# Kernel optimization log

Measured on AMD Instinct MI355X. Metric: run time of the kernel, lower is better.

## Reference

```python
import jax, jax.numpy as jnp
import numpy as np

N_QUBITS = 4
N_LAYERS = 2
BATCH = 262144


def _apply_ry(psi, theta, wire):
    # psi: (B, 2,2,2,2) real statevector; theta: scalar or (B,)
    c = jnp.reshape(jnp.cos(theta * 0.5), (-1, 1, 1, 1))
    s = jnp.reshape(jnp.sin(theta * 0.5), (-1, 1, 1, 1))
    psi = jnp.moveaxis(psi, wire + 1, 1)
    a, b = psi[:, 0], psi[:, 1]
    psi = jnp.stack([c * a - s * b, s * a + c * b], axis=1)
    return jnp.moveaxis(psi, 1, wire + 1)


def _apply_cnot(psi, ctrl, tgt):
    # flip target amplitude where control bit is 1
    psi = jnp.moveaxis(psi, (ctrl + 1, tgt + 1), (1, 2))
    psi = psi.at[:, 1].set(psi[:, 1, ::-1])
    return jnp.moveaxis(psi, (1, 2), (ctrl + 1, tgt + 1))


def _circuit(encoded, q_params):
    # Batched 4-qubit statevector sim (RY/CNOT are real matrices -> real psi).
    B = encoded.shape[0]
    psi = jnp.zeros((B, 2 ** N_QUBITS), encoded.dtype).at[:, 0].set(1.0)
    psi = psi.reshape((B,) + (2,) * N_QUBITS)  # wire 0 = most significant axis
    for w in range(N_QUBITS):
        psi = _apply_ry(psi, encoded[:, w], w)
    for layer in range(N_LAYERS):
        for i in range(N_QUBITS - 1):
            psi = _apply_cnot(psi, i, i + 1)
        psi = _apply_cnot(psi, N_QUBITS - 1, 0)  # ring closure (n_qubits > 2)
        for i in range(N_QUBITS):
            psi = _apply_ry(psi, q_params[layer * N_QUBITS + i], i)
    p = psi * psi  # probabilities
    zs = []
    for w in range(N_QUBITS):
        pw = jnp.moveaxis(p, w + 1, 1).reshape(B, 2, -1)
        zs.append(pw[:, 0].sum(-1) - pw[:, 1].sum(-1))  # <Z_w>
    return jnp.stack(zs, axis=-1)  # (B, 4)


def setup_inputs() -> dict:
    key = jax.random.key(0)
    ks = jax.random.split(key, 10)
    f32 = jnp.float32
    state = jax.random.normal(ks[0], (BATCH, 64), dtype=f32)
    # state_encoder: Linear(64,32) -> ReLU -> Linear(32,4) -> Tanh
    W1 = jax.random.normal(ks[1], (32, 64), dtype=f32) / np.sqrt(64.0)
    b1 = jnp.zeros((32,), f32)
    W2 = jax.random.normal(ks[2], (N_QUBITS, 32), dtype=f32) / np.sqrt(32.0)
    b2 = jnp.zeros((N_QUBITS,), f32)
    q_params = jax.random.normal(ks[3], (N_LAYERS * N_QUBITS,), dtype=f32) * 0.1
    # q_value_head: Linear(4,32) -> ReLU -> Linear(32,16) -> Tanh
    H1 = jax.random.normal(ks[4], (32, N_QUBITS), dtype=f32) / np.sqrt(float(N_QUBITS))
    c1 = jnp.zeros((32,), f32)
    H2 = jax.random.normal(ks[5], (16, 32), dtype=f32) / np.sqrt(32.0)
    c2 = jnp.zeros((16,), f32)
    return {"state": state, "W1": W1, "b1": b1, "W2": W2, "b2": b2,
            "q_params": q_params, "H1": H1, "c1": c1, "H2": H2, "c2": c2}


def reference(state, W1, b1, W2, b2, q_params, H1, c1, H2, c2):
    B = state.shape[0]
    x = state.reshape(B, -1)
    h = jax.nn.relu(x @ W1.T + b1)
    encoded = jnp.tanh(h @ W2.T + b2)            # (B, 4) rotation angles
    qf = _circuit(encoded, q_params)             # (B, 4) PauliZ expectations
    h2 = jax.nn.relu(qf @ H1.T + c1)
    q_values = jnp.tanh(h2 @ H2.T + c2)          # (B, 16)
    return q_values.reshape(B, 4, 4)
```

## Files before the change

kernel.cpp:

```cpp
#include <hip/hip_runtime.h>
#include <hip/hip_bf16.h>

#define TPB 256
#define BATCH 262144
#define S 34

typedef __fp16   fp16x2  __attribute__((ext_vector_type(2)));
typedef _Float16 half8_t __attribute__((ext_vector_type(8)));
typedef float    f32x4   __attribute__((ext_vector_type(4)));

#define WAVE_LDS_FENCE() asm volatile("s_waitcnt lgkmcnt(0)" ::: "memory")

__device__ __forceinline__ float fast_tanh(float x) {
    float ax = fabsf(x);
    float e  = __expf(-2.0f * ax);
    float t  = (1.0f - e) * __builtin_amdgcn_rcpf(1.0f + e);
    return copysignf(t, x);
}

template <int MASK>
__device__ __forceinline__ void ry_gate(float* psi, float c, float s) {
#pragma unroll
    for (int i = 0; i < 16; i++) {
        if (!(i & MASK)) {
            float a = psi[i], b = psi[i | MASK];
            psi[i]        = c * a - s * b;
            psi[i | MASK] = s * a + c * b;
        }
    }
}

template <int CM, int TM>
__device__ __forceinline__ void cnot_gate(float* psi) {
#pragma unroll
    for (int i = 0; i < 16; i++) {
        if ((i & CM) && !(i & TM)) {
            float t = psi[i];
            psi[i] = psi[i | TM];
            psi[i | TM] = t;
        }
    }
}

__device__ __forceinline__ half8_t cvt8(float4 a, float4 b) {
    fp16x2 p0 = __builtin_amdgcn_cvt_pkrtz(a.x, a.y);
    fp16x2 p1 = __builtin_amdgcn_cvt_pkrtz(a.z, a.w);
    fp16x2 p2 = __builtin_amdgcn_cvt_pkrtz(b.x, b.y);
    fp16x2 p3 = __builtin_amdgcn_cvt_pkrtz(b.z, b.w);
    half8_t r;
    r[0] = (_Float16)p0[0]; r[1] = (_Float16)p0[1];
    r[2] = (_Float16)p1[0]; r[3] = (_Float16)p1[1];
    r[4] = (_Float16)p2[0]; r[5] = (_Float16)p2[1];
    r[6] = (_Float16)p3[0]; r[7] = (_Float16)p3[1];
    return r;
}

__global__ __launch_bounds__(TPB, 4) void qnet_kernel(
    const float* __restrict__ state,
    const float* __restrict__ W1, const float* __restrict__ b1,
    const float* __restrict__ W2, const float* __restrict__ b2,
    const float* __restrict__ qp,
    const float* __restrict__ H1, const float* __restrict__ c1,
    const float* __restrict__ H2, const float* __restrict__ c2,
    float* __restrict__ out)
{
    __shared__ float sh[4 * 64 * S];

    const int tid  = threadIdx.x;
    const int lane = tid & 63;
    const int wv   = tid >> 6;
    const int l15  = lane & 15;
    const int lq   = lane >> 4;
    const int rowBase = blockIdx.x * TPB + wv * 64;
    float* hb = sh + wv * 64 * S;

    float4 xa[4][2], xb[4][2];
#pragma unroll
    for (int mt = 0; mt < 4; mt++) {
        const float* p0 = state + (size_t)(rowBase + 16 * mt + l15) * 64 + lq * 8;
#pragma unroll
        for (int kt = 0; kt < 2; kt++) {
            xa[mt][kt] = *(const float4*)(p0 + 32 * kt);
            xb[mt][kt] = *(const float4*)(p0 + 32 * kt + 4);
        }
    }

    half8_t bW1[2][2];
#pragma unroll
    for (int u = 0; u < 2; u++)
#pragma unroll
        for (int kt = 0; kt < 2; kt++) {
            const float* p = W1 + (16 * u + l15) * 64 + 32 * kt + lq * 8;
            bW1[u][kt] = cvt8(*(const float4*)p, *(const float4*)(p + 4));
        }
    const float bias0 = b1[l15];
    const float bias1 = b1[16 + l15];

    f32x4 acc[4][2];
#pragma unroll
    for (int mt = 0; mt < 4; mt++)
#pragma unroll
        for (int u = 0; u < 2; u++)
#pragma unroll
            for (int r = 0; r < 4; r++) acc[mt][u][r] = 0.0f;

#pragma unroll
    for (int kt = 0; kt < 2; kt++) {
#pragma unroll
        for (int mt = 0; mt < 4; mt++) {
            half8_t a = cvt8(xa[mt][kt], xb[mt][kt]);
            acc[mt][0] = __builtin_amdgcn_mfma_f32_16x16x32_f16(a, bW1[0][kt], acc[mt][0], 0, 0, 0);
            acc[mt][1] = __builtin_amdgcn_mfma_f32_16x16x32_f16(a, bW1[1][kt], acc[mt][1], 0, 0, 0);
        }
    }

#pragma unroll
    for (int mt = 0; mt < 4; mt++)
#pragma unroll
        for (int r = 0; r < 4; r++) {
            int row = 16 * mt + 4 * lq + r;
            hb[row * S + l15]      = fmaxf(acc[mt][0][r] + bias0, 0.0f);
            hb[row * S + 16 + l15] = fmaxf(acc[mt][1][r] + bias1, 0.0f);
        }
    WAVE_LDS_FENCE();

    float h[32];
    {
        const float2* hr = reinterpret_cast<const float2*>(hb + lane * S);
#pragma unroll
        for (int j = 0; j < 16; j++) { float2 v = hr[j]; h[2 * j] = v.x; h[2 * j + 1] = v.y; }
    }

    float e[4];
#pragma unroll
    for (int w = 0; w < 4; w++) {
        float a = b2[w];
#pragma unroll
        for (int k = 0; k < 32; k++) a = fmaf(h[k], W2[w * 32 + k], a);
        e[w] = fast_tanh(a);
    }

    float qf[4];
    {
        float psi[16];
#pragma unroll
        for (int i = 0; i < 16; i++) psi[i] = 0.0f;
        psi[0] = 1.0f;

        float s, c;
        __sincosf(0.5f * e[0], &s, &c); ry_gate<8>(psi, c, s);
        __sincosf(0.5f * e[1], &s, &c); ry_gate<4>(psi, c, s);
        __sincosf(0.5f * e[2], &s, &c); ry_gate<2>(psi, c, s);
        __sincosf(0.5f * e[3], &s, &c); ry_gate<1>(psi, c, s);

#pragma unroll
        for (int layer = 0; layer < 2; layer++) {
            cnot_gate<8, 4>(psi);
            cnot_gate<4, 2>(psi);
            cnot_gate<2, 1>(psi);
            cnot_gate<1, 8>(psi);
#pragma unroll
            for (int i = 0; i < 4; i++) {
                float s2, c2v;
                __sincosf(0.5f * qp[layer * 4 + i], &s2, &c2v);
                if (i == 0) ry_gate<8>(psi, c2v, s2);
                if (i == 1) ry_gate<4>(psi, c2v, s2);
                if (i == 2) ry_gate<2>(psi, c2v, s2);
                if (i == 3) ry_gate<1>(psi, c2v, s2);
            }
        }

        float p[16];
#pragma unroll
        for (int i = 0; i < 16; i++) p[i] = psi[i] * psi[i];
#pragma unroll
        for (int w = 0; w < 4; w++) {
            const int m = 8 >> w;
            float z = 0.0f;
#pragma unroll
            for (int i = 0; i < 16; i++) z += (i & m) ? -p[i] : p[i];
            qf[w] = z;
        }
    }

    float h2[32];
#pragma unroll
    for (int j = 0; j < 32; j++) {
        float a = c1[j];
        a = fmaf(qf[0], H1[j * 4 + 0], a);
        a = fmaf(qf[1], H1[j * 4 + 1], a);
        a = fmaf(qf[2], H1[j * 4 + 2], a);
        a = fmaf(qf[3], H1[j * 4 + 3], a);
        h2[j] = fmaxf(a, 0.0f);
    }

    WAVE_LDS_FENCE();
    {
        float2* hw = reinterpret_cast<float2*>(hb + lane * S);
#pragma unroll
        for (int j = 0; j < 16; j++) hw[j] = make_float2(h2[2 * j], h2[2 * j + 1]);
    }
    WAVE_LDS_FENCE();

    half8_t bH2;
    {
        const float* p = H2 + l15 * 32 + lq * 8;
        bH2 = cvt8(*(const float4*)p, *(const float4*)(p + 4));
    }

    f32x4 acc2[4];
#pragma unroll
    for (int mt = 0; mt < 4; mt++)
#pragma unroll
        for (int r = 0; r < 4; r++) acc2[mt][r] = 0.0f;

#pragma unroll
    for (int mt = 0; mt < 4; mt++) {
        const float2* q = reinterpret_cast<const float2*>(hb + (16 * mt + l15) * S + lq * 8);
        float2 a0 = q[0], a1 = q[1], a2 = q[2], a3 = q[3];
        half8_t a = cvt8(make_float4(a0.x, a0.y, a1.x, a1.y),
                         make_float4(a2.x, a2.y, a3.x, a3.y));
        acc2[mt] = __builtin_amdgcn_mfma_f32_16x16x32_f16(a, bH2, acc2[mt], 0, 0, 0);
    }

    const float cc = c2[l15];
#pragma unroll
    for (int mt = 0; mt < 4; mt++)
#pragma unroll
        for (int r = 0; r < 4; r++) {
            int row = rowBase + 16 * mt + 4 * lq + r;
            out[(size_t)row * 16 + l15] = fast_tanh(acc2[mt][r] + cc);
        }
}

extern "C" void kernel_launch(void* const* d_in, const int* in_sizes, int n_in,
                              void* d_out, int out_size, void* d_ws, size_t ws_size,
                              hipStream_t stream) {
    const float* state = (const float*)d_in[0];
    const float* W1    = (const float*)d_in[1];
    const float* b1    = (const float*)d_in[2];
    const float* W2    = (const float*)d_in[3];
    const float* b2    = (const float*)d_in[4];
    const float* qp    = (const float*)d_in[5];
    const float* H1    = (const float*)d_in[6];
    const float* c1    = (const float*)d_in[7];
    const float* H2    = (const float*)d_in[8];
    const float* c2    = (const float*)d_in[9];
    float* out = (float*)d_out;

    const int blocks = BATCH / TPB;
    qnet_kernel<<<blocks, TPB, 0, stream>>>(state, W1, b1, W2, b2, qp,
                                            H1, c1, H2, c2, out);
}
```

Baseline: 118.7 us.

## Halve rows per wave, precompute circuit sincos in LDS, raise occupancy

```diff
diff --git a/kernel.cpp b/kernel.cpp
--- a/kernel.cpp
+++ b/kernel.cpp
@@ -55,7 +55,7 @@
     return r;
 }
 
-__global__ __launch_bounds__(TPB, 4) void qnet_kernel(
+__global__ __launch_bounds__(TPB, 6) void qnet_kernel(
     const float* __restrict__ state,
     const float* __restrict__ W1, const float* __restrict__ b1,
     const float* __restrict__ W2, const float* __restrict__ b2,
@@ -64,25 +64,32 @@
     const float* __restrict__ H2, const float* __restrict__ c2,
     float* __restrict__ out)
 {
-    __shared__ float sh[4 * 64 * S];
+    __shared__ float sh[4 * 32 * S];
+    __shared__ float sQc[8], sQs[8];
 
     const int tid  = threadIdx.x;
     const int lane = tid & 63;
     const int wv   = tid >> 6;
     const int l15  = lane & 15;
     const int lq   = lane >> 4;
-    const int rowBase = blockIdx.x * TPB + wv * 64;
-    float* hb = sh + wv * 64 * S;
-
-    float4 xa[4][2], xb[4][2];
-#pragma unroll
-    for (int mt = 0; mt < 4; mt++) {
+    const int rowBase = blockIdx.x * 128 + wv * 32;
+    float* hb = sh + wv * 32 * S;
+
+    if (tid < 8) {
+        float s, c;
+        __sincosf(0.5f * qp[tid], &s, &c);
+        sQs[tid] = s; sQc[tid] = c;
+    }
+    __syncthreads();
+
+    half8_t aX[2][2];
+#pragma unroll
+    for (int mt = 0; mt < 2; mt++) {
         const float* p0 = state + (size_t)(rowBase + 16 * mt + l15) * 64 + lq * 8;
 #pragma unroll
-        for (int kt = 0; kt < 2; kt++) {
-            xa[mt][kt] = *(const float4*)(p0 + 32 * kt);
-            xb[mt][kt] = *(const float4*)(p0 + 32 * kt + 4);
-        }
+        for (int kt = 0; kt < 2; kt++)
+            aX[mt][kt] = cvt8(*(const float4*)(p0 + 32 * kt),
+                              *(const float4*)(p0 + 32 * kt + 4));
     }
 
     half8_t bW1[2][2];
@@ -96,26 +103,24 @@
     const float bias0 = b1[l15];
     const float bias1 = b1[16 + l15];
 
-    f32x4 acc[4][2];
-#pragma unroll
-    for (int mt = 0; mt < 4; mt++)
+    f32x4 acc[2][2];
+#pragma unroll
+    for (int mt = 0; mt < 2; mt++)
 #pragma unroll
         for (int u = 0; u < 2; u++)
 #pragma unroll
             for (int r = 0; r < 4; r++) acc[mt][u][r] = 0.0f;
 
 #pragma unroll
-    for (int kt = 0; kt < 2; kt++) {
-#pragma unroll
-        for (int mt = 0; mt < 4; mt++) {
-            half8_t a = cvt8(xa[mt][kt], xb[mt][kt]);
-            acc[mt][0] = __builtin_amdgcn_mfma_f32_16x16x32_f16(a, bW1[0][kt], acc[mt][0], 0, 0, 0);
-            acc[mt][1] = __builtin_amdgcn_mfma_f32_16x16x32_f16(a, bW1[1][kt], acc[mt][1], 0, 0, 0);
-        }
-    }
-
-#pragma unroll
-    for (int mt = 0; mt < 4; mt++)
+    for (int kt = 0; kt < 2; kt++)
+#pragma unroll
+        for (int mt = 0; mt < 2; mt++) {
+            acc[mt][0] = __builtin_amdgcn_mfma_f32_16x16x32_f16(aX[mt][kt], bW1[0][kt], acc[mt][0], 0, 0, 0);
+            acc[mt][1] = __builtin_amdgcn_mfma_f32_16x16x32_f16(aX[mt][kt], bW1[1][kt], acc[mt][1], 0, 0, 0);
+        }
+
+#pragma unroll
+    for (int mt = 0; mt < 2; mt++)
 #pragma unroll
         for (int r = 0; r < 4; r++) {
             int row = 16 * mt + 4 * lq + r;
@@ -124,24 +129,21 @@
         }
     WAVE_LDS_FENCE();
 
-    float h[32];
-    {
+    if (lane < 32) {
+        float h[32];
         const float2* hr = reinterpret_cast<const float2*>(hb + lane * S);
 #pragma unroll
         for (int j = 0; j < 16; j++) { float2 v = hr[j]; h[2 * j] = v.x; h[2 * j + 1] = v.y; }
-    }
-
-    float e[4];
-#pragma unroll
-    for (int w = 0; w < 4; w++) {
-        float a = b2[w];
-#pragma unroll
-        for (int k = 0; k < 32; k++) a = fmaf(h[k], W2[w * 32 + k], a);
-        e[w] = fast_tanh(a);
-    }
-
-    float qf[4];
-    {
+
+        float e[4];
+#pragma unroll
+        for (int w = 0; w < 4; w++) {
+            float a = b2[w];
+#pragma unroll
+            for (int k = 0; k < 32; k++) a = fmaf(h[k], W2[w * 32 + k], a);
+            e[w] = fast_tanh(a);
+        }
+
         float psi[16];
 #pragma unroll
         for (int i = 0; i < 16; i++) psi[i] = 0.0f;
@@ -159,20 +161,16 @@
             cnot_gate<4, 2>(psi);
             cnot_gate<2, 1>(psi);
             cnot_gate<1, 8>(psi);
-#pragma unroll
-            for (int i = 0; i < 4; i++) {
-                float s2, c2v;
-                __sincosf(0.5f * qp[layer * 4 + i], &s2, &c2v);
-                if (i == 0) ry_gate<8>(psi, c2v, s2);
-                if (i == 1) ry_gate<4>(psi, c2v, s2);
-                if (i == 2) ry_gate<2>(psi, c2v, s2);
-                if (i == 3) ry_gate<1>(psi, c2v, s2);
-            }
+            ry_gate<8>(psi, sQc[layer * 4 + 0], sQs[layer * 4 + 0]);
+            ry_gate<4>(psi, sQc[layer * 4 + 1], sQs[layer * 4 + 1]);
+            ry_gate<2>(psi, sQc[layer * 4 + 2], sQs[layer * 4 + 2]);
+            ry_gate<1>(psi, sQc[layer * 4 + 3], sQs[layer * 4 + 3]);
         }
 
         float p[16];
 #pragma unroll
         for (int i = 0; i < 16; i++) p[i] = psi[i] * psi[i];
+        float qf[4];
 #pragma unroll
         for (int w = 0; w < 4; w++) {
             const int m = 8 >> w;
@@ -181,24 +179,21 @@
             for (int i = 0; i < 16; i++) z += (i & m) ? -p[i] : p[i];
             qf[w] = z;
         }
-    }
-
-    float h2[32];
-#pragma unroll
-    for (int j = 0; j < 32; j++) {
-        float a = c1[j];
-        a = fmaf(qf[0], H1[j * 4 + 0], a);
-        a = fmaf(qf[1], H1[j * 4 + 1], a);
-        a = fmaf(qf[2], H1[j * 4 + 2], a);
-        a = fmaf(qf[3], H1[j * 4 + 3], a);
-        h2[j] = fmaxf(a, 0.0f);
-    }
-
-    WAVE_LDS_FENCE();
-    {
+
         float2* hw = reinterpret_cast<float2*>(hb + lane * S);
 #pragma unroll
-        for (int j = 0; j < 16; j++) hw[j] = make_float2(h2[2 * j], h2[2 * j + 1]);
+        for (int jj = 0; jj < 16; jj++) {
+            float a0 = c1[2 * jj], a1 = c1[2 * jj + 1];
+            a0 = fmaf(qf[0], H1[(2 * jj) * 4 + 0], a0);
+            a0 = fmaf(qf[1], H1[(2 * jj) * 4 + 1], a0);
+            a0 = fmaf(qf[2], H1[(2 * jj) * 4 + 2], a0);
+            a0 = fmaf(qf[3], H1[(2 * jj) * 4 + 3], a0);
+            a1 = fmaf(qf[0], H1[(2 * jj + 1) * 4 + 0], a1);
+            a1 = fmaf(qf[1], H1[(2 * jj + 1) * 4 + 1], a1);
+            a1 = fmaf(qf[2], H1[(2 * jj + 1) * 4 + 2], a1);
+            a1 = fmaf(qf[3], H1[(2 * jj + 1) * 4 + 3], a1);
+            hw[jj] = make_float2(fmaxf(a0, 0.0f), fmaxf(a1, 0.0f));
+        }
     }
     WAVE_LDS_FENCE();
 
@@ -208,14 +203,14 @@
         bH2 = cvt8(*(const float4*)p, *(const float4*)(p + 4));
     }
 
-    f32x4 acc2[4];
-#pragma unroll
-    for (int mt = 0; mt < 4; mt++)
+    f32x4 acc2[2];
+#pragma unroll
+    for (int mt = 0; mt < 2; mt++)
 #pragma unroll
         for (int r = 0; r < 4; r++) acc2[mt][r] = 0.0f;
 
 #pragma unroll
-    for (int mt = 0; mt < 4; mt++) {
+    for (int mt = 0; mt < 2; mt++) {
         const float2* q = reinterpret_cast<const float2*>(hb + (16 * mt + l15) * S + lq * 8);
         float2 a0 = q[0], a1 = q[1], a2 = q[2], a3 = q[3];
         half8_t a = cvt8(make_float4(a0.x, a0.y, a1.x, a1.y),
@@ -225,7 +220,7 @@
 
     const float cc = c2[l15];
 #pragma unroll
-    for (int mt = 0; mt < 4; mt++)
+    for (int mt = 0; mt < 2; mt++)
 #pragma unroll
         for (int r = 0; r < 4; r++) {
             int row = rowBase + 16 * mt + 4 * lq + r;
@@ -248,7 +243,7 @@
     const float* c2    = (const float*)d_in[9];
     float* out = (float*)d_out;
 
-    const int blocks = BATCH / TPB;
+    const int blocks = BATCH / 128;
     qnet_kernel<<<blocks, TPB, 0, stream>>>(state, W1, b1, W2, b2, qp,
                                             H1, c1, H2, c2, out);
 }
```

New measurement: 123.4 us. 1.04x slower.
